# Kernel tuning notes

Measured on AMD Instinct MI355X. Metric: run time of the kernel, lower is better.

## Reference

```python
import jax, jax.numpy as jnp
import numpy as np

B, T, SD, CD = 2048, 512, 8, 8
H = 64 + SD  # control_rnn_size + state_dim = 72


def setup_inputs() -> dict:
    key = jax.random.key(0)
    ks = jax.random.split(key, 16)
    s = 0.05
    inp = {
        "x": jax.random.normal(ks[0], (B, SD), jnp.float32),
        "rnn_input": jax.random.normal(ks[1], (B, T, CD + 1), jnp.float32),
        "deltas": jax.random.uniform(ks[2], (B, T, 1), jnp.float32),
        "h_lens": jax.random.randint(ks[3], (B,), T // 2, T + 1, jnp.int32),
        "W_ih": s * jax.random.normal(ks[4], (4 * H, CD + 1), jnp.float32),
        "W_hh": s * jax.random.normal(ks[5], (4 * H, H), jnp.float32),
        "b_ih": jnp.zeros((4 * H,), jnp.float32),
        "b_hh": jnp.zeros((4 * H,), jnp.float32),
        "enc_W1": s * jax.random.normal(ks[6], (256, SD), jnp.float32),
        "enc_b1": jnp.zeros((256,), jnp.float32),
        "enc_W2": s * jax.random.normal(ks[7], (256, 256), jnp.float32),
        "enc_b2": jnp.zeros((256,), jnp.float32),
        "enc_W3": s * jax.random.normal(ks[8], (64, 256), jnp.float32),
        "enc_b3": jnp.zeros((64,), jnp.float32),
        "dec_W1": s * jax.random.normal(ks[9], (288, H), jnp.float32),
        "dec_b1": jnp.zeros((288,), jnp.float32),
        "dec_W2": s * jax.random.normal(ks[10], (288, 288), jnp.float32),
        "dec_b2": jnp.zeros((288,), jnp.float32),
        "dec_W3": s * jax.random.normal(ks[11], (SD, 288), jnp.float32),
        "dec_b3": jnp.zeros((SD,), jnp.float32),
    }
    return inp


def _mlp(z, Ws_bs):
    # Linear->Tanh repeated, final Linear without activation
    *hidden, (Wf, bf) = Ws_bs
    for W, b in hidden:
        z = jnp.tanh(z @ W.T + b)
    return z @ Wf.T + bf


def _lstm(rnn_input, h0, c0, W_ih, W_hh, b_ih, b_hh):
    # rnn_input: [B,T,I]; h0,c0: [B,H]. PyTorch gate order: i,f,g,o.
    x_proj = rnn_input @ W_ih.T + (b_ih + b_hh)  # [B,T,4H]

    def step(carry, xt):
        h, c = carry
        gates = xt + h @ W_hh.T
        i, f, g, o = jnp.split(gates, 4, axis=-1)
        i, f, o = jax.nn.sigmoid(i), jax.nn.sigmoid(f), jax.nn.sigmoid(o)
        c = f * c + i * jnp.tanh(g)
        h = o * jnp.tanh(c)
        return (h, c), h

    _, hs = jax.lax.scan(step, (h0, c0), jnp.swapaxes(x_proj, 0, 1))
    return jnp.swapaxes(hs, 0, 1)  # [B,T,H]


def reference(x, rnn_input, deltas, h_lens, W_ih, W_hh, b_ih, b_hh,
              enc_W1, enc_b1, enc_W2, enc_b2, enc_W3, enc_b3,
              dec_W1, dec_b1, dec_W2, dec_b2, dec_W3, dec_b3):
    h0 = _mlp(x, [(enc_W1, enc_b1), (enc_W2, enc_b2), (enc_W3, enc_b3)])  # [B,64]
    h0_stack = jnp.concatenate([x, h0], axis=1)  # [B,H]
    c0 = jnp.zeros_like(h0_stack)
    h = _lstm(rnn_input, h0_stack, c0, W_ih, W_hh, b_ih, b_hh)  # [B,T,H]
    # roll by 1 with h0 in slot 0
    h_shift = jnp.concatenate([h0_stack[:, None, :], h[:, :-1, :]], axis=1)
    encoded = (1.0 - deltas) * h_shift + deltas * h  # [B,T,H]
    dec_in = encoded[jnp.arange(encoded.shape[0]), h_lens - 1, :]  # [B,H]
    out = _mlp(dec_in, [(dec_W1, dec_b1), (dec_W2, dec_b2), (dec_W3, dec_b3)])
    return out[:, :SD]
```

## Files before the change

kernel.cpp:

```cpp
#include <hip/hip_runtime.h>
#include <cstdint>

#define HH 72
#define NR 4
#define NTH 512
#define NBLK 512
#define TT 512

typedef __attribute__((ext_vector_type(8))) _Float16 half8;
typedef __attribute__((ext_vector_type(4))) float f32x4;

#if __has_builtin(__builtin_amdgcn_exp2f)
#define EXP2(x) __builtin_amdgcn_exp2f(x)
#else
#define EXP2(x) exp2f(x)
#endif
#if __has_builtin(__builtin_amdgcn_rcpf)
#define RCP(x) __builtin_amdgcn_rcpf(x)
#else
#define RCP(x) (1.0f/(x))
#endif

__device__ __forceinline__ float fsig(float x) {
  float e = EXP2(x * -1.442695040888963f);
  return RCP(1.0f + e);
}
__device__ __forceinline__ float ftanh(float x) {
  float e = EXP2(x * -2.885390081777927f);
  return fmaf(2.0f, RCP(1.0f + e), -1.0f);
}

__device__ __forceinline__ unsigned short f2h(float v) {
  union { _Float16 h; unsigned short u; } cv;
  cv.h = (_Float16)v;
  return cv.u;
}

__device__ __forceinline__ int bidx(int k, int m) {
  return ((k >> 5)*4 + ((k >> 3) & 3))*128 + m*8 + (k & 7);
}

__device__ __forceinline__ float swz4(float v) { return __int_as_float(__builtin_amdgcn_ds_swizzle(__float_as_int(v), 0x101F)); }
__device__ __forceinline__ float swz8(float v) { return __int_as_float(__builtin_amdgcn_ds_swizzle(__float_as_int(v), 0x201F)); }

__device__ __forceinline__ float cellUpd(float ig, float fg, float gg, float og, float& c) {
  c = fmaf(fsig(fg), c, fsig(ig)*ftanh(gg));
  return fsig(og)*ftanh(c);
}

#define FMA4(A, W_, P_) { \
  const float4 _fa = *(const float4*)(P_); \
  A[0] = fmaf((W_), _fa.x, A[0]); A[1] = fmaf((W_), _fa.y, A[1]); \
  A[2] = fmaf((W_), _fa.z, A[2]); A[3] = fmaf((W_), _fa.w, A[3]); }

__global__ void cfm_sort(const int* __restrict__ h_lens, int* __restrict__ perm) {
  __shared__ int hist[257];
  __shared__ int offs[257];
  const int t = threadIdx.x;
  for (int i = t; i < 257; i += 256) hist[i] = 0;
  __syncthreads();
  for (int i = t; i < 2048; i += 256) {
    int bkt = min(max(h_lens[i] - 256, 0), 256);
    atomicAdd(&hist[bkt], 1);
  }
  __syncthreads();
  if (t == 0) { int s = 0; for (int i = 0; i < 257; ++i) { offs[i] = s; s += hist[i]; } }
  __syncthreads();
  for (int i = t; i < 2048; i += 256) {
    int bkt = min(max(h_lens[i] - 256, 0), 256);
    int pos = atomicAdd(&offs[bkt], 1);
    perm[pos] = i;
  }
}

__global__ __launch_bounds__(NTH, 4)
void cfm_main(const float* __restrict__ x, const float* __restrict__ rnn,
              const float* __restrict__ deltas, const int* __restrict__ h_lens,
              const float* __restrict__ W_ih, const float* __restrict__ W_hh,
              const float* __restrict__ b_ih, const float* __restrict__ b_hh,
              const float* __restrict__ eW1, const float* __restrict__ eb1,
              const float* __restrict__ eW2, const float* __restrict__ eb2,
              const float* __restrict__ eW3, const float* __restrict__ eb3,
              const float* __restrict__ dW1, const float* __restrict__ db1,
              const float* __restrict__ dW2, const float* __restrict__ db2,
              const float* __restrict__ dW3, const float* __restrict__ db3,
              const int* __restrict__ perm, float* __restrict__ out)
{
  __shared__ __align__(16) unsigned short hF[2][1536];
  __shared__ __align__(16) float gS[1152];
  __shared__ __align__(16) float rnnS[1152];
  __shared__ __align__(16) float snapP[NR][HH];
  __shared__ __align__(16) float snapC[NR][HH];
  __shared__ __align__(16) float hS[HH][NR];
  __shared__ __align__(16) float xS[8][NR];
  __shared__ int brS[NR];
  __shared__ int idxS[NR];
  __shared__ float dS[NR];

  const int t  = threadIdx.x;
  const int bb = blockIdx.x;
  const int pgrp = (bb < 256) ? bb : (767 - bb);

  for (int i = t; i < 1536; i += NTH) ((unsigned*)hF)[i] = 0;

  if (t < NR) {
    int row = perm ? perm[pgrp*NR + t] : (pgrp*NR + t);
    brS[t]  = row;
    idxS[t] = h_lens[row] - 1;
  }
  __syncthreads();

  int maxIdx = idxS[0];
  #pragma unroll
  for (int r = 1; r < NR; ++r) maxIdx = max(maxIdx, idxS[r]);

  const int lane = t & 63;
  const int wv   = t >> 6;
  const int col  = lane & 15;
  const int q_a  = lane >> 4;
  const int base = (wv < 2) ? wv*3 : 6 + (wv - 2)*2;
  const int nt   = (wv < 2) ? 3 : 2;
  const int g    = col >> 2;
  const int c    = col & 3;
  const bool act = (g < nt);
  const int cidxE = idxS[c];
  const int uA = 4*(base + (act ? g : 0)) + q_a;
  float cstA = 0.f;

  if (t < 32) { int r = t >> 3, k = t & 7; xS[k][r] = x[brS[r]*8 + k]; }
  __syncthreads();

  float* z1S = gS;
  if (t < 256) {
    float acc[NR];
    float b = eb1[t];
    #pragma unroll
    for (int r = 0; r < NR; ++r) acc[r] = b;
    #pragma unroll
    for (int k = 0; k < 8; ++k) { float w = eW1[t*8 + k]; FMA4(acc, w, &xS[k][0]); }
    #pragma unroll
    for (int r = 0; r < NR; ++r) z1S[t*4 + r] = ftanh(acc[r]);
  }
  __syncthreads();
  float* z2S = rnnS;
  if (t < 256) {
    float acc[NR];
    float b = eb2[t];
    #pragma unroll
    for (int r = 0; r < NR; ++r) acc[r] = b;
    const float4* w4 = (const float4*)(eW2 + t*256);
    #pragma unroll 4
    for (int k4 = 0; k4 < 64; ++k4) {
      float4 w = w4[k4];
      FMA4(acc, w.x, z1S + (4*k4+0)*4);
      FMA4(acc, w.y, z1S + (4*k4+1)*4);
      FMA4(acc, w.z, z1S + (4*k4+2)*4);
      FMA4(acc, w.w, z1S + (4*k4+3)*4);
    }
    #pragma unroll
    for (int r = 0; r < NR; ++r) z2S[t*4 + r] = ftanh(acc[r]);
  }
  __syncthreads();
  if (t < 64) {
    float acc[NR];
    float b = eb3[t];
    #pragma unroll
    for (int r = 0; r < NR; ++r) acc[r] = b;
    const float4* w4 = (const float4*)(eW3 + t*256);
    #pragma unroll 4
    for (int k4 = 0; k4 < 64; ++k4) {
      float4 w = w4[k4];
      FMA4(acc, w.x, z2S + (4*k4+0)*4);
      FMA4(acc, w.y, z2S + (4*k4+1)*4);
      FMA4(acc, w.z, z2S + (4*k4+2)*4);
      FMA4(acc, w.w, z2S + (4*k4+3)*4);
    }
    int u = 8 + t;
    #pragma unroll
    for (int r = 0; r < NR; ++r) hF[0][bidx(u, r)] = f2h(acc[r]);
  } else if (t < 96) {
    int tt2 = t - 64; int r = tt2 >> 3, k = tt2 & 7;
    hF[0][bidx(k, r)] = f2h(xS[k][r]);
  }

  half8 Af[3][3];
  f32x4 biasq[3];
  #pragma unroll
  for (int i = 0; i < 3; ++i) {
    int ii = (i < nt) ? i : 0;
    int u = 4*(base + ii) + q_a;
    biasq[i].x = b_ih[u]       + b_hh[u];
    biasq[i].y = b_ih[72 + u]  + b_hh[72 + u];
    biasq[i].z = b_ih[144 + u] + b_hh[144 + u];
    biasq[i].w = b_ih[216 + u] + b_hh[216 + u];
    int nprime = (base + ii)*16 + col;
    int srcrow = (nprime & 3)*72 + (nprime >> 2);
    #pragma unroll
    for (int kt = 0; kt < 3; ++kt) {
      union { unsigned short u16[8]; half8 h; } cw;
      #pragma unroll
      for (int j = 0; j < 8; ++j) {
        int k = kt*32 + q_a*8 + j;
        float v = 0.f;
        if (k < 72)      v = W_hh[srcrow*HH + k];
        else if (k < 81) v = W_ih[srcrow*9 + (k - 72)];
        cw.u16[j] = f2h(v);
      }
      Af[i][kt] = cw.h;
    }
  }

  int step = 0;
  int par = 0;
  __syncthreads();
  for (int chunk = 0; chunk*32 <= maxIdx; ++chunk) {
    for (int e = t; e < 1152; e += NTH) {
      int r = e / 288, pos = e % 288;
      int tc = pos / 9, kk = pos - tc*9;
      rnnS[tc*36 + r*9 + kk] = rnn[brS[r]*4608 + chunk*288 + pos];
    }
    __syncthreads();
    if (t < 36) {
      int r = t / 9, kk = t - r*9;
      hF[par][bidx(72 + kk, r)] = f2h(rnnS[t]);
    }
    __syncthreads();
    int lim = min(31, maxIdx - chunk*32);
    for (int tc = 0; tc <= lim; ++tc, ++step) {
      const int np = par ^ 1;
      half8 bf[3];
      #pragma unroll
      for (int kt = 0; kt < 3; ++kt) {
        int rb = (kt*4 + q_a)*128 + col*8;
        bf[kt] = *(const half8*)&hF[par][rb];
      }
      f32x4 acc[3];
      #pragma unroll
      for (int i = 0; i < 3; ++i) acc[i] = biasq[i];
      #pragma unroll
      for (int kt = 0; kt < 3; ++kt) {
        #pragma unroll
        for (int i = 0; i < 3; ++i) {
          if (i < nt) {
            acc[i] = __builtin_amdgcn_mfma_f32_16x16x32_f16(Af[i][kt], bf[kt], acc[i], 0, 0, 0);
          }
        }
      }
      float s1x = swz4(acc[1].x), s1y = swz4(acc[1].y), s1z = swz4(acc[1].z), s1w = swz4(acc[1].w);
      float s2x = swz8(acc[2].x), s2y = swz8(acc[2].y), s2z = swz8(acc[2].z), s2w = swz8(acc[2].w);
      if (act) {
        float ig = (g == 0) ? acc[0].x : (g == 1) ? s1x : s2x;
        float fg = (g == 0) ? acc[0].y : (g == 1) ? s1y : s2y;
        float gg = (g == 0) ? acc[0].z : (g == 1) ? s1z : s2z;
        float og = (g == 0) ? acc[0].w : (g == 1) ? s1w : s2w;
        float hv = cellUpd(ig, fg, gg, og, cstA);
        hF[np][bidx(uA, c)] = f2h(hv);
        if (step == cidxE - 1) snapP[c][uA] = hv;
        if (step == cidxE)     snapC[c][uA] = hv;
      }
      if (tc < 31 && t < 36) {
        int r = t / 9, kk = t - r*9;
        hF[np][bidx(72 + kk, r)] = f2h(rnnS[(tc+1)*36 + t]);
      }
      __syncthreads();
      par = np;
    }
  }

  if (t < NR) dS[t] = deltas[brS[t]*TT + idxS[t]];
  __syncthreads();

  for (int p = t; p < 288; p += NTH) {
    int u = p % 72, r = p / 72;
    float d = dS[r];
    float sp = snapP[r][u], sc = snapC[r][u];
    hS[u][r] = fmaf(d, sc - sp, sp);
  }
  __syncthreads();

  float* d1S = rnnS;
  for (int n = t; n < 288; n += NTH) {
    float acc[NR];
    float b = db1[n];
    #pragma unroll
    for (int r = 0; r < NR; ++r) acc[r] = b;
    const float4* w4 = (const float4*)(dW1 + n*HH);
    #pragma unroll 2
    for (int k4 = 0; k4 < 18; ++k4) {
      float4 w = w4[k4];
      FMA4(acc, w.x, &hS[4*k4+0][0]);
      FMA4(acc, w.y, &hS[4*k4+1][0]);
      FMA4(acc, w.z, &hS[4*k4+2][0]);
      FMA4(acc, w.w, &hS[4*k4+3][0]);
    }
    #pragma unroll
    for (int r = 0; r < NR; ++r) d1S[n*4 + r] = ftanh(acc[r]);
  }
  __syncthreads();

  float* d2S = gS;
  for (int n = t; n < 288; n += NTH) {
    float acc[NR];
    float b = db2[n];
    #pragma unroll
    for (int r = 0; r < NR; ++r) acc[r] = b;
    const float4* w4 = (const float4*)(dW2 + n*288);
    #pragma unroll 4
    for (int k4 = 0; k4 < 72; ++k4) {
      float4 w = w4[k4];
      FMA4(acc, w.x, d1S + (4*k4+0)*4);
      FMA4(acc, w.y, d1S + (4*k4+1)*4);
      FMA4(acc, w.z, d1S + (4*k4+2)*4);
      FMA4(acc, w.w, d1S + (4*k4+3)*4);
    }
    #pragma unroll
    for (int r = 0; r < NR; ++r) d2S[n*4 + r] = ftanh(acc[r]);
  }
  __syncthreads();

  if (t < 32) {
    int o = t & 7, r = t >> 3;
    float acc3 = db3[o];
    const float* wr = dW3 + o*288;
    #pragma unroll 4
    for (int k = 0; k < 288; ++k) acc3 = fmaf(wr[k], d2S[k*4 + r], acc3);
    out[brS[r]*8 + o] = acc3;
  }
}

extern "C" void kernel_launch(void* const* d_in, const int* in_sizes, int n_in,
                              void* d_out, int out_size, void* d_ws, size_t ws_size,
                              hipStream_t stream) {
  const float* x      = (const float*)d_in[0];
  const float* rnn    = (const float*)d_in[1];
  const float* deltas = (const float*)d_in[2];
  const int*   h_lens = (const int*)  d_in[3];
  const float* W_ih   = (const float*)d_in[4];
  const float* W_hh   = (const float*)d_in[5];
  const float* b_ih   = (const float*)d_in[6];
  const float* b_hh   = (const float*)d_in[7];
  const float* eW1    = (const float*)d_in[8];
  const float* eb1    = (const float*)d_in[9];
  const float* eW2    = (const float*)d_in[10];
  const float* eb2    = (const float*)d_in[11];
  const float* eW3    = (const float*)d_in[12];
  const float* eb3    = (const float*)d_in[13];
  const float* dW1    = (const float*)d_in[14];
  const float* db1    = (const float*)d_in[15];
  const float* dW2    = (const float*)d_in[16];
  const float* db2    = (const float*)d_in[17];
  const float* dW3    = (const float*)d_in[18];
  const float* db3    = (const float*)d_in[19];
  float* out = (float*)d_out;

  int* perm = nullptr;
  if (ws_size >= 2048 * sizeof(int)) {
    perm = (int*)d_ws;
    cfm_sort<<<1, 256, 0, stream>>>(h_lens, perm);
  }
  cfm_main<<<NBLK, NTH, 0, stream>>>(x, rnn, deltas, h_lens, W_ih, W_hh, b_ih, b_hh,
                                     eW1, eb1, eW2, eb2, eW3, eb3,
                                     dW1, db1, dW2, db2, dW3, db3,
                                     perm, out);
}
```

Baseline: 437.1 us.

## Process eight batch rows per block with nine waves and register-prefetched inputs

Each block now handles 8 sequences instead of 4, using 9 waves that each own two 16-column gate tiles. This removes the cross-lane swizzles and idle lanes of the old uneven 3/2 tile split. The next chunk of rnn_input is prefetched into registers while the current chunk runs, and the time loop is unrolled by two with fixed buffer parity. The block count halves to 256 and the launch-bound occupancy drops to 2, so fewer, larger blocks each run a longer sequential recurrence, and the pairing of short and long groups across blocks is removed.

Result: faster. 355.6 us (-18.7%).

```diff
diff --git a/kernel.cpp b/kernel.cpp
--- a/kernel.cpp
+++ b/kernel.cpp
@@ -2,9 +2,9 @@
 #include <cstdint>
 
 #define HH 72
-#define NR 4
-#define NTH 512
-#define NBLK 512
+#define NR 8
+#define NTH 576
+#define NBLK 256
 #define TT 512
 
 typedef __attribute__((ext_vector_type(8))) _Float16 half8;
@@ -37,11 +37,8 @@
 }
 
 __device__ __forceinline__ int bidx(int k, int m) {
-  return ((k >> 5)*4 + ((k >> 3) & 3))*128 + m*8 + (k & 7);
-}
-
-__device__ __forceinline__ float swz4(float v) { return __int_as_float(__builtin_amdgcn_ds_swizzle(__float_as_int(v), 0x101F)); }
-__device__ __forceinline__ float swz8(float v) { return __int_as_float(__builtin_amdgcn_ds_swizzle(__float_as_int(v), 0x201F)); }
+  return ((k >> 5)*4 + ((k >> 3) & 3))*64 + m*8 + (k & 7);
+}
 
 __device__ __forceinline__ float cellUpd(float ig, float fg, float gg, float og, float& c) {
   c = fmaf(fsig(fg), c, fsig(ig)*ftanh(gg));
@@ -73,7 +70,7 @@
   }
 }
 
-__global__ __launch_bounds__(NTH, 4)
+__global__ __launch_bounds__(NTH, 2)
 void cfm_main(const float* __restrict__ x, const float* __restrict__ rnn,
               const float* __restrict__ deltas, const int* __restrict__ h_lens,
               const float* __restrict__ W_ih, const float* __restrict__ W_hh,
@@ -86,25 +83,24 @@
               const float* __restrict__ dW3, const float* __restrict__ db3,
               const int* __restrict__ perm, float* __restrict__ out)
 {
-  __shared__ __align__(16) unsigned short hF[2][1536];
-  __shared__ __align__(16) float gS[1152];
-  __shared__ __align__(16) float rnnS[1152];
+  __shared__ __align__(16) unsigned short hF[2][768];
+  __shared__ __align__(16) float gS[2304];
+  __shared__ __align__(16) float rnnS[2336];
   __shared__ __align__(16) float snapP[NR][HH];
   __shared__ __align__(16) float snapC[NR][HH];
-  __shared__ __align__(16) float hS[HH][NR];
-  __shared__ __align__(16) float xS[8][NR];
+  __shared__ __align__(16) float hS[HH*NR];
+  __shared__ __align__(16) float xS[8*NR];
   __shared__ int brS[NR];
   __shared__ int idxS[NR];
   __shared__ float dS[NR];
 
   const int t  = threadIdx.x;
   const int bb = blockIdx.x;
-  const int pgrp = (bb < 256) ? bb : (767 - bb);
-
-  for (int i = t; i < 1536; i += NTH) ((unsigned*)hF)[i] = 0;
+
+  for (int i = t; i < 768; i += NTH) ((unsigned*)hF)[i] = 0;
 
   if (t < NR) {
-    int row = perm ? perm[pgrp*NR + t] : (pgrp*NR + t);
+    int row = perm ? perm[bb*NR + t] : (bb*NR + t);
     brS[t]  = row;
     idxS[t] = h_lens[row] - 1;
   }
@@ -118,82 +114,95 @@
   const int wv   = t >> 6;
   const int col  = lane & 15;
   const int q_a  = lane >> 4;
-  const int base = (wv < 2) ? wv*3 : 6 + (wv - 2)*2;
-  const int nt   = (wv < 2) ? 3 : 2;
-  const int g    = col >> 2;
-  const int c    = col & 3;
-  const bool act = (g < nt);
-  const int cidxE = idxS[c];
-  const int uA = 4*(base + (act ? g : 0)) + q_a;
+  const int cL   = col & 7;
+  const int gHi  = col >> 3;
+  const int uA   = 4*(2*wv + gHi) + q_a;
+  const int cidxE  = idxS[cL];
+  const int cidxm1 = cidxE - 1;
+  const int ibA  = bidx(uA, cL);
+  const int bOff0 = (0*4 + q_a)*64 + cL*8;
+  const int bOff1 = (1*4 + q_a)*64 + cL*8;
+  const int bOff2 = (2*4 + q_a)*64 + cL*8;
   float cstA = 0.f;
 
-  if (t < 32) { int r = t >> 3, k = t & 7; xS[k][r] = x[brS[r]*8 + k]; }
+  const int pfR = t / 72;
+  const int pfP = t - pfR*72;
+  const float4* rnnRow = (const float4*)(rnn + (size_t)brS[pfR]*4608) + pfP;
+  float4 pf = rnnRow[0];
+
+  const bool doXt = (t < 72);
+  int xtDst = 0, xtSrc = 0;
+  if (doXt) {
+    int rX = t / 9, kX = t - rX*9;
+    xtDst = bidx(72 + kX, rX);
+    xtSrc = rX*292 + kX;
+  }
+
+  if (t < 64) { int r = t >> 3, k = t & 7; xS[k*8 + r] = x[brS[r]*8 + k]; }
   __syncthreads();
 
   float* z1S = gS;
-  if (t < 256) {
-    float acc[NR];
-    float b = eb1[t];
-    #pragma unroll
-    for (int r = 0; r < NR; ++r) acc[r] = b;
-    #pragma unroll
-    for (int k = 0; k < 8; ++k) { float w = eW1[t*8 + k]; FMA4(acc, w, &xS[k][0]); }
-    #pragma unroll
-    for (int r = 0; r < NR; ++r) z1S[t*4 + r] = ftanh(acc[r]);
+  if (t < 512) {
+    int n = t >> 1, rh = (t & 1)*4;
+    float acc[4];
+    float b = eb1[n];
+    acc[0]=b; acc[1]=b; acc[2]=b; acc[3]=b;
+    #pragma unroll
+    for (int k = 0; k < 8; ++k) { float w = eW1[n*8 + k]; FMA4(acc, w, &xS[k*8 + rh]); }
+    #pragma unroll
+    for (int j = 0; j < 4; ++j) z1S[n*8 + rh + j] = ftanh(acc[j]);
   }
   __syncthreads();
   float* z2S = rnnS;
-  if (t < 256) {
-    float acc[NR];
-    float b = eb2[t];
-    #pragma unroll
-    for (int r = 0; r < NR; ++r) acc[r] = b;
-    const float4* w4 = (const float4*)(eW2 + t*256);
+  if (t < 512) {
+    int n = t >> 1, rh = (t & 1)*4;
+    float acc[4];
+    float b = eb2[n];
+    acc[0]=b; acc[1]=b; acc[2]=b; acc[3]=b;
+    const float4* w4 = (const float4*)(eW2 + n*256);
     #pragma unroll 4
     for (int k4 = 0; k4 < 64; ++k4) {
       float4 w = w4[k4];
-      FMA4(acc, w.x, z1S + (4*k4+0)*4);
-      FMA4(acc, w.y, z1S + (4*k4+1)*4);
-      FMA4(acc, w.z, z1S + (4*k4+2)*4);
-      FMA4(acc, w.w, z1S + (4*k4+3)*4);
-    }
-    #pragma unroll
-    for (int r = 0; r < NR; ++r) z2S[t*4 + r] = ftanh(acc[r]);
-  }
-  __syncthreads();
-  if (t < 64) {
-    float acc[NR];
-    float b = eb3[t];
-    #pragma unroll
-    for (int r = 0; r < NR; ++r) acc[r] = b;
-    const float4* w4 = (const float4*)(eW3 + t*256);
+      FMA4(acc, w.x, &z1S[(4*k4+0)*8 + rh]);
+      FMA4(acc, w.y, &z1S[(4*k4+1)*8 + rh]);
+      FMA4(acc, w.z, &z1S[(4*k4+2)*8 + rh]);
+      FMA4(acc, w.w, &z1S[(4*k4+3)*8 + rh]);
+    }
+    #pragma unroll
+    for (int j = 0; j < 4; ++j) z2S[n*8 + rh + j] = ftanh(acc[j]);
+  }
+  __syncthreads();
+  if (t < 128) {
+    int o = t >> 1, rh = (t & 1)*4;
+    float acc[4];
+    float b = eb3[o];
+    acc[0]=b; acc[1]=b; acc[2]=b; acc[3]=b;
+    const float4* w4 = (const float4*)(eW3 + o*256);
     #pragma unroll 4
     for (int k4 = 0; k4 < 64; ++k4) {
       float4 w = w4[k4];
-      FMA4(acc, w.x, z2S + (4*k4+0)*4);
-      FMA4(acc, w.y, z2S + (4*k4+1)*4);
-      FMA4(acc, w.z, z2S + (4*k4+2)*4);
-      FMA4(acc, w.w, z2S + (4*k4+3)*4);
-    }
-    int u = 8 + t;
-    #pragma unroll
-    for (int r = 0; r < NR; ++r) hF[0][bidx(u, r)] = f2h(acc[r]);
-  } else if (t < 96) {
-    int tt2 = t - 64; int r = tt2 >> 3, k = tt2 & 7;
-    hF[0][bidx(k, r)] = f2h(xS[k][r]);
-  }
-
-  half8 Af[3][3];
-  f32x4 biasq[3];
+      FMA4(acc, w.x, &z2S[(4*k4+0)*8 + rh]);
+      FMA4(acc, w.y, &z2S[(4*k4+1)*8 + rh]);
+      FMA4(acc, w.z, &z2S[(4*k4+2)*8 + rh]);
+      FMA4(acc, w.w, &z2S[(4*k4+3)*8 + rh]);
+    }
+    #pragma unroll
+    for (int j = 0; j < 4; ++j) hF[0][bidx(8 + o, rh + j)] = f2h(acc[j]);
+  } else if (t < 192) {
+    int tt2 = t - 128; int r = tt2 >> 3, k = tt2 & 7;
+    hF[0][bidx(k, r)] = f2h(xS[k*8 + r]);
+  }
+
+  half8 Af[2][3];
+  f32x4 biasq[2];
   #pragma unroll
-  for (int i = 0; i < 3; ++i) {
-    int ii = (i < nt) ? i : 0;
-    int u = 4*(base + ii) + q_a;
+  for (int i = 0; i < 2; ++i) {
+    int u = 4*(2*wv + i) + q_a;
     biasq[i].x = b_ih[u]       + b_hh[u];
     biasq[i].y = b_ih[72 + u]  + b_hh[72 + u];
     biasq[i].z = b_ih[144 + u] + b_hh[144 + u];
     biasq[i].w = b_ih[216 + u] + b_hh[216 + u];
-    int nprime = (base + ii)*16 + col;
+    int nprime = (2*wv + i)*16 + col;
     int srcrow = (nprime & 3)*72 + (nprime >> 2);
     #pragma unroll
     for (int kt = 0; kt < 3; ++kt) {
@@ -210,120 +219,102 @@
     }
   }
 
+#define STEP(PAR) { \
+    const unsigned short* hb = &hF[PAR][0]; \
+    unsigned short* hn = &hF[(PAR) ^ 1][0]; \
+    half8 bf0 = *(const half8*)(hb + bOff0); \
+    half8 bf1 = *(const half8*)(hb + bOff1); \
+    half8 bf2 = *(const half8*)(hb + bOff2); \
+    f32x4 a0 = __builtin_amdgcn_mfma_f32_16x16x32_f16(Af[0][0], bf0, biasq[0], 0, 0, 0); \
+    f32x4 a1 = __builtin_amdgcn_mfma_f32_16x16x32_f16(Af[1][0], bf0, biasq[1], 0, 0, 0); \
+    a0 = __builtin_amdgcn_mfma_f32_16x16x32_f16(Af[0][1], bf1, a0, 0, 0, 0); \
+    a1 = __builtin_amdgcn_mfma_f32_16x16x32_f16(Af[1][1], bf1, a1, 0, 0, 0); \
+    a0 = __builtin_amdgcn_mfma_f32_16x16x32_f16(Af[0][2], bf2, a0, 0, 0, 0); \
+    a1 = __builtin_amdgcn_mfma_f32_16x16x32_f16(Af[1][2], bf2, a1, 0, 0, 0); \
+    float ig = gHi ? a1.x : a0.x; \
+    float fg = gHi ? a1.y : a0.y; \
+    float gg = gHi ? a1.z : a0.z; \
+    float og = gHi ? a1.w : a0.w; \
+    float hv = cellUpd(ig, fg, gg, og, cstA); \
+    hn[ibA] = f2h(hv); \
+    if (step == cidxm1) snapP[cL][uA] = hv; \
+    if (step == cidxE)  snapC[cL][uA] = hv; \
+    if (doXt && tc < 31) hn[xtDst] = f2h(rnnS[xtSrc + (tc + 1)*9]); \
+    __syncthreads(); \
+    ++tc; ++step; }
+
   int step = 0;
-  int par = 0;
-  __syncthreads();
   for (int chunk = 0; chunk*32 <= maxIdx; ++chunk) {
-    for (int e = t; e < 1152; e += NTH) {
-      int r = e / 288, pos = e % 288;
-      int tc = pos / 9, kk = pos - tc*9;
-      rnnS[tc*36 + r*9 + kk] = rnn[brS[r]*4608 + chunk*288 + pos];
-    }
     __syncthreads();
-    if (t < 36) {
-      int r = t / 9, kk = t - r*9;
-      hF[par][bidx(72 + kk, r)] = f2h(rnnS[t]);
-    }
+    *(float4*)&rnnS[pfR*292 + pfP*4] = pf;
+    if ((chunk + 1)*32 <= maxIdx) pf = rnnRow[(chunk + 1)*72];
     __syncthreads();
-    int lim = min(31, maxIdx - chunk*32);
-    for (int tc = 0; tc <= lim; ++tc, ++step) {
-      const int np = par ^ 1;
-      half8 bf[3];
-      #pragma unroll
-      for (int kt = 0; kt < 3; ++kt) {
-        int rb = (kt*4 + q_a)*128 + col*8;
-        bf[kt] = *(const half8*)&hF[par][rb];
-      }
-      f32x4 acc[3];
-      #pragma unroll
-      for (int i = 0; i < 3; ++i) acc[i] = biasq[i];
-      #pragma unroll
-      for (int kt = 0; kt < 3; ++kt) {
-        #pragma unroll
-        for (int i = 0; i < 3; ++i) {
-          if (i < nt) {
-            acc[i] = __builtin_amdgcn_mfma_f32_16x16x32_f16(Af[i][kt], bf[kt], acc[i], 0, 0, 0);
-          }
-        }
-      }
-      float s1x = swz4(acc[1].x), s1y = swz4(acc[1].y), s1z = swz4(acc[1].z), s1w = swz4(acc[1].w);
-      float s2x = swz8(acc[2].x), s2y = swz8(acc[2].y), s2z = swz8(acc[2].z), s2w = swz8(acc[2].w);
-      if (act) {
-        float ig = (g == 0) ? acc[0].x : (g == 1) ? s1x : s2x;
-        float fg = (g == 0) ? acc[0].y : (g == 1) ? s1y : s2y;
-        float gg = (g == 0) ? acc[0].z : (g == 1) ? s1z : s2z;
-        float og = (g == 0) ? acc[0].w : (g == 1) ? s1w : s2w;
-        float hv = cellUpd(ig, fg, gg, og, cstA);
-        hF[np][bidx(uA, c)] = f2h(hv);
-        if (step == cidxE - 1) snapP[c][uA] = hv;
-        if (step == cidxE)     snapC[c][uA] = hv;
-      }
-      if (tc < 31 && t < 36) {
-        int r = t / 9, kk = t - r*9;
-        hF[np][bidx(72 + kk, r)] = f2h(rnnS[(tc+1)*36 + t]);
-      }
-      __syncthreads();
-      par = np;
-    }
-  }
+    if (doXt) hF[0][xtDst] = f2h(rnnS[xtSrc]);
+    __syncthreads();
+    const int lim = min(31, maxIdx - chunk*32);
+    int tc = 0;
+    while (tc + 1 <= lim) { STEP(0) STEP(1) }
+    if (tc <= lim) { STEP(0) }
+  }
+#undef STEP
 
   if (t < NR) dS[t] = deltas[brS[t]*TT + idxS[t]];
   __syncthreads();
 
-  for (int p = t; p < 288; p += NTH) {
-    int u = p % 72, r = p / 72;
+  {
+    int u = t % 72, r = t / 72;
     float d = dS[r];
     float sp = snapP[r][u], sc = snapC[r][u];
-    hS[u][r] = fmaf(d, sc - sp, sp);
+    hS[u*8 + r] = fmaf(d, sc - sp, sp);
   }
   __syncthreads();
 
   float* d1S = rnnS;
-  for (int n = t; n < 288; n += NTH) {
-    float acc[NR];
+  {
+    int n = t >> 1, rh = (t & 1)*4;
+    float acc[4];
     float b = db1[n];
-    #pragma unroll
-    for (int r = 0; r < NR; ++r) acc[r] = b;
+    acc[0]=b; acc[1]=b; acc[2]=b; acc[3]=b;
     const float4* w4 = (const float4*)(dW1 + n*HH);
     #pragma unroll 2
     for (int k4 = 0; k4 < 18; ++k4) {
       float4 w = w4[k4];
-      FMA4(acc, w.x, &hS[4*k4+0][0]);
-      FMA4(acc, w.y, &hS[4*k4+1][0]);
-      FMA4(acc, w.z, &hS[4*k4+2][0]);
-      FMA4(acc, w.w, &hS[4*k4+3][0]);
-    }
-    #pragma unroll
-    for (int r = 0; r < NR; ++r) d1S[n*4 + r] = ftanh(acc[r]);
+      FMA4(acc, w.x, &hS[(4*k4+0)*8 + rh]);
+      FMA4(acc, w.y, &hS[(4*k4+1)*8 + rh]);
+      FMA4(acc, w.z, &hS[(4*k4+2)*8 + rh]);
+      FMA4(acc, w.w, &hS[(4*k4+3)*8 + rh]);
+    }
+    #pragma unroll
+    for (int j = 0; j < 4; ++j) d1S[n*8 + rh + j] = ftanh(acc[j]);
   }
   __syncthreads();
 
   float* d2S = gS;
-  for (int n = t; n < 288; n += NTH) {
-    float acc[NR];
+  {
+    int n = t >> 1, rh = (t & 1)*4;
+    float acc[4];
     float b = db2[n];
-    #pragma unroll
-    for (int r = 0; r < NR; ++r) acc[r] = b;
+    acc[0]=b; acc[1]=b; acc[2]=b; acc[3]=b;
     const float4* w4 = (const float4*)(dW2 + n*288);
     #pragma unroll 4
     for (int k4 = 0; k4 < 72; ++k4) {
       float4 w = w4[k4];
-      FMA4(acc, w.x, d1S + (4*k4+0)*4);
-      FMA4(acc, w.y, d1S + (4*k4+1)*4);
-      FMA4(acc, w.z, d1S + (4*k4+2)*4);
-      FMA4(acc, w.w, d1S + (4*k4+3)*4);
-    }
-    #pragma unroll
-    for (int r = 0; r < NR; ++r) d2S[n*4 + r] = ftanh(acc[r]);
-  }
-  __syncthreads();
-
-  if (t < 32) {
+      FMA4(acc, w.x, &d1S[(4*k4+0)*8 + rh]);
+      FMA4(acc, w.y, &d1S[(4*k4+1)*8 + rh]);
+      FMA4(acc, w.z, &d1S[(4*k4+2)*8 + rh]);
+      FMA4(acc, w.w, &d1S[(4*k4+3)*8 + rh]);
+    }
+    #pragma unroll
+    for (int j = 0; j < 4; ++j) d2S[n*8 + rh + j] = ftanh(acc[j]);
+  }
+  __syncthreads();
+
+  if (t < 64) {
     int o = t & 7, r = t >> 3;
     float acc3 = db3[o];
     const float* wr = dW3 + o*288;
     #pragma unroll 4
-    for (int k = 0; k < 288; ++k) acc3 = fmaf(wr[k], d2S[k*4 + r], acc3);
+    for (int k = 0; k < 288; ++k) acc3 = fmaf(wr[k], d2S[k*8 + r], acc3);
     out[brS[r]*8 + o] = acc3;
   }
 }
```
